# Kernel optimization log

Measured on AMD Instinct MI355X. Metric: run time of the kernel, lower is better.

Reference implementation:

```python
import jax, jax.numpy as jnp
import numpy as np

D_MODEL = 1024
N_HEADS = 16
D_K = D_MODEL // N_HEADS
D_FF = 4096
EPS = 1e-6


def setup_inputs() -> dict:
    key = jax.random.key(0)
    ks = jax.random.split(key, 12)
    s = 1.0 / np.sqrt(D_MODEL)
    inp = {
        "x": jax.random.normal(ks[0], (4, 2048, D_MODEL), jnp.float32),
        "src_mask": jnp.ones((4, 1, 1, 2048), jnp.int32),
        "Wq": jax.random.normal(ks[1], (D_MODEL, D_MODEL), jnp.float32) * s,
        "bq": jnp.zeros((D_MODEL,), jnp.float32),
        "Wk": jax.random.normal(ks[2], (D_MODEL, D_MODEL), jnp.float32) * s,
        "bk": jnp.zeros((D_MODEL,), jnp.float32),
        "Wv": jax.random.normal(ks[3], (D_MODEL, D_MODEL), jnp.float32) * s,
        "bv": jnp.zeros((D_MODEL,), jnp.float32),
        "Wo": jax.random.normal(ks[4], (D_MODEL, D_MODEL), jnp.float32) * s,
        "bo": jnp.zeros((D_MODEL,), jnp.float32),
        "W1": jax.random.normal(ks[5], (D_MODEL, D_FF), jnp.float32) * s,
        "b1": jnp.zeros((D_FF,), jnp.float32),
        "W2": jax.random.normal(ks[6], (D_FF, D_MODEL), jnp.float32) * (1.0 / np.sqrt(D_FF)),
        "b2": jnp.zeros((D_MODEL,), jnp.float32),
        # scalar LayerNormalization params (alpha=ones(1), bias=zeros(1)) for the 2 residual norms
        "ln1_alpha": jnp.ones((1,), jnp.float32),
        "ln1_bias": jnp.zeros((1,), jnp.float32),
        "ln2_alpha": jnp.ones((1,), jnp.float32),
        "ln2_bias": jnp.zeros((1,), jnp.float32),
    }
    return inp


def _layernorm(x, alpha, bias):
    # matches torch: mean + std (unbiased, ddof=1), (x-mean)/(std+eps)
    mean = jnp.mean(x, axis=-1, keepdims=True)
    std = jnp.std(x, axis=-1, keepdims=True, ddof=1)
    return alpha * ((x - mean) / (std + EPS)) + bias


def _mha(x, mask, Wq, bq, Wk, bk, Wv, bv, Wo, bo):
    B, S, _ = x.shape
    q = (x @ Wq + bq).reshape(B, S, N_HEADS, D_K).transpose(0, 2, 1, 3)
    k = (x @ Wk + bk).reshape(B, S, N_HEADS, D_K).transpose(0, 2, 1, 3)
    v = (x @ Wv + bv).reshape(B, S, N_HEADS, D_K).transpose(0, 2, 1, 3)
    scores = jnp.einsum("bhqd,bhkd->bhqk", q, k) / jnp.sqrt(jnp.float32(D_K))
    scores = jnp.where(mask == 0, jnp.float32(-1e9), scores)
    attn = jax.nn.softmax(scores, axis=-1)
    ctx = jnp.einsum("bhqk,bhkd->bhqd", attn, v)
    ctx = ctx.transpose(0, 2, 1, 3).reshape(B, S, D_MODEL)
    return ctx @ Wo + bo


def reference(x, src_mask, Wq, bq, Wk, bk, Wv, bv, Wo, bo, W1, b1, W2, b2,
              ln1_alpha, ln1_bias, ln2_alpha, ln2_bias):
    # pre-norm residual 1: self-attention
    h = _layernorm(x, ln1_alpha, ln1_bias)
    x = x + _mha(h, src_mask, Wq, bq, Wk, bk, Wv, bv, Wo, bo)
    # pre-norm residual 2: FFN
    h = _layernorm(x, ln2_alpha, ln2_bias)
    ff = jax.nn.relu(h @ W1 + b1) @ W2 + b2
    return x + ff
```

## Files before the change

### kernel.cpp

```cpp
#include <hip/hip_runtime.h>

typedef __attribute__((ext_vector_type(8))) short v8s;
typedef __attribute__((ext_vector_type(8))) unsigned short v8u;
typedef __attribute__((ext_vector_type(4))) unsigned short v4u;
typedef __attribute__((ext_vector_type(4))) float f32x4;

#define DEV __device__ __forceinline__

DEV unsigned short f2bf(float f) {
  union { float f; unsigned u; } v; v.f = f;
  unsigned r = v.u + 0x7fffu + ((v.u >> 16) & 1u);
  return (unsigned short)(r >> 16);
}

DEV float fexp2(float x) {
  float r; asm("v_exp_f32 %0, %1" : "=v"(r) : "v"(x)); return r;
}

DEV void gload16(const unsigned short* g, unsigned short* l) {
  __builtin_amdgcn_global_load_lds(
      (const __attribute__((address_space(1))) unsigned int*)g,
      (__attribute__((address_space(3))) unsigned int*)l, 16, 0, 0);
}

#define SL2E 0.1803368801111204f

__global__ __launch_bounds__(256) void ln_kernel(
    const float* __restrict__ x, unsigned short* __restrict__ h,
    const float* __restrict__ alpha, const float* __restrict__ beta)
{
  int row = blockIdx.x;
  int tid = threadIdx.x;
  const float4* xr = reinterpret_cast<const float4*>(x + (size_t)row * 1024);
  float4 v = xr[tid];
  float s  = v.x + v.y + v.z + v.w;
  float ss = v.x * v.x + v.y * v.y + v.z * v.z + v.w * v.w;
#pragma unroll
  for (int off = 1; off < 64; off <<= 1) {
    s  += __shfl_xor(s, off);
    ss += __shfl_xor(ss, off);
  }
  __shared__ float ps[4][2];
  int wid = tid >> 6, lane = tid & 63;
  if (lane == 0) { ps[wid][0] = s; ps[wid][1] = ss; }
  __syncthreads();
  s  = ps[0][0] + ps[1][0] + ps[2][0] + ps[3][0];
  ss = ps[0][1] + ps[1][1] + ps[2][1] + ps[3][1];
  float mean = s * (1.0f / 1024.0f);
  float var  = (ss - 1024.0f * mean * mean) * (1.0f / 1023.0f);
  float inv  = 1.0f / (sqrtf(fmaxf(var, 0.0f)) + 1e-6f);
  float a = alpha[0], b = beta[0];
  v4u o;
  o[0] = f2bf(a * ((v.x - mean) * inv) + b);
  o[1] = f2bf(a * ((v.y - mean) * inv) + b);
  o[2] = f2bf(a * ((v.z - mean) * inv) + b);
  o[3] = f2bf(a * ((v.w - mean) * inv) + b);
  *reinterpret_cast<v4u*>(h + (size_t)row * 1024 + tid * 4) = o;
}

__global__ __launch_bounds__(256) void transpose_convert(
    const float* __restrict__ W, unsigned short* __restrict__ Wt, int K, int N)
{
  __shared__ float t[32][33];
  int n0 = blockIdx.x * 32, k0 = blockIdx.y * 32;
  int tx = threadIdx.x, ty = threadIdx.y;
#pragma unroll
  for (int i = 0; i < 4; ++i)
    t[ty + i * 8][tx] = W[(size_t)(k0 + ty + i * 8) * N + n0 + tx];
  __syncthreads();
#pragma unroll
  for (int i = 0; i < 4; ++i)
    Wt[(size_t)(n0 + ty + i * 8) * K + k0 + tx] = f2bf(t[tx][ty + i * 8]);
}

#define BUF_ELEMS ((128 + 256) * 64)

DEV void stage_part(const unsigned short* Aptr, const unsigned short* Bptr,
                    unsigned short* buf, int K, int part, int wid, int lane)
{
  {
    int d = (part * 8 + wid) * 64 + lane;
    int r = d >> 3, p = d & 7;
    gload16(Aptr + (size_t)r * K + 8 * (p ^ (r & 7)),
            buf + (size_t)(part * 8 + wid) * 512);
  }
#pragma unroll
  for (int j = 0; j < 2; ++j) {
    int ib = part * 2 + j;
    int d = (ib * 8 + wid) * 64 + lane;
    int r = d >> 3, p = d & 7;
    gload16(Bptr + (size_t)r * K + 8 * (p ^ (r & 7)),
            buf + 128 * 64 + (size_t)(ib * 8 + wid) * 512);
  }
}

__global__ __launch_bounds__(512, 1) void gemm_qkv(
    const unsigned short* __restrict__ A, const unsigned short* __restrict__ Bt,
    const float* __restrict__ bq, const float* __restrict__ bk2,
    const float* __restrict__ bv,
    unsigned short* __restrict__ oq, unsigned short* __restrict__ ok2,
    unsigned short* __restrict__ ov, int M, int N, int K)
{
  __shared__ unsigned short lds[3 * BUF_ELEMS];

  int nbx = M >> 7, nwg = gridDim.x;
  int lin = blockIdx.x;
  int qq = nwg >> 3, rr = nwg & 7;
  int xcd = lin & 7, idx = lin >> 3;
  int swz = (xcd < rr ? xcd * (qq + 1) : rr * (qq + 1) + (xcd - rr) * qq) + idx;
  int bx = swz % nbx, by = swz / nbx;

  int tid = threadIdx.x, lane = tid & 63, wid = tid >> 6;
  int g = lane >> 4, c0 = lane & 15;
  int rowBase = bx * 128, colBase = by * 256;

  const unsigned short* Ab = A  + (size_t)rowBase * K;
  const unsigned short* Bb = Bt + (size_t)colBase * K;
  int NT = K >> 6;

  f32x4 acc[8][2];
#pragma unroll
  for (int m = 0; m < 8; ++m)
#pragma unroll
    for (int n = 0; n < 2; ++n) acc[m][n] = (f32x4){0.f, 0.f, 0.f, 0.f};

  stage_part(Ab, Bb, lds, K, 0, wid, lane);
  stage_part(Ab, Bb, lds, K, 1, wid, lane);
  stage_part(Ab + 64, Bb + 64, lds + BUF_ELEMS, K, 0, wid, lane);
  stage_part(Ab + 64, Bb + 64, lds + BUF_ELEMS, K, 1, wid, lane);
  asm volatile("s_waitcnt vmcnt(6)" ::: "memory");
  __builtin_amdgcn_s_barrier();
  asm volatile("" ::: "memory");

  int cur = 0;
  for (int t = 0; t < NT; ++t) {
    const char* Abuf = (const char*)(lds + cur * BUF_ELEMS);
    const char* Bbuf = Abuf + 128 * 128;
    int nxt2 = cur + 2; if (nxt2 >= 3) nxt2 -= 3;
    unsigned short* sbuf = lds + nxt2 * BUF_ELEMS;
    bool doStage = (t + 2 < NT);
    int ks_ = (t + 2) << 6;

#pragma unroll
    for (int ph = 0; ph < 2; ++ph) {
      v8s af[8], bfr[2];
#pragma unroll
      for (int m = 0; m < 8; ++m) {
        int row = m * 16 + c0;
        af[m] = *reinterpret_cast<const v8s*>(
            Abuf + row * 128 + ((ph * 64 + g * 16) ^ ((row & 7) << 4)));
      }
#pragma unroll
      for (int n = 0; n < 2; ++n) {
        int row = wid * 32 + n * 16 + c0;
        bfr[n] = *reinterpret_cast<const v8s*>(
            Bbuf + row * 128 + ((ph * 64 + g * 16) ^ ((row & 7) << 4)));
      }

      if (doStage) stage_part(Ab + ks_, Bb + ks_, sbuf, K, ph, wid, lane);

      __builtin_amdgcn_s_setprio(1);
#pragma unroll
      for (int m = 0; m < 8; ++m)
#pragma unroll
        for (int n = 0; n < 2; ++n)
          acc[m][n] = __builtin_amdgcn_mfma_f32_16x16x32_bf16(
              af[m], bfr[n], acc[m][n], 0, 0, 0);
      __builtin_amdgcn_s_setprio(0);
    }

    if (doStage)            asm volatile("s_waitcnt vmcnt(6)" ::: "memory");
    else if (t + 1 < NT)    asm volatile("s_waitcnt vmcnt(0)" ::: "memory");
    __builtin_amdgcn_sched_barrier(0);
    __builtin_amdgcn_s_barrier();
    asm volatile("" ::: "memory");
    cur = cur + 1; if (cur >= 3) cur -= 3;
  }

#pragma unroll
  for (int mf = 0; mf < 8; ++mf) {
#pragma unroll
    for (int nf = 0; nf < 2; ++nf) {
#pragma unroll
      for (int r = 0; r < 4; ++r) {
        int row = rowBase + mf * 16 + g * 4 + r;
        int col = colBase + wid * 32 + nf * 16 + c0;
        int sect = colBase >> 10;
        int cs = col & 1023;
        const float* bp = sect == 0 ? bq : (sect == 1 ? bk2 : bv);
        float v = acc[mf][nf][r] + bp[cs];
        int hh = cs >> 6, d = cs & 63;
        int b = row >> 11, sI = row & 2047;
        size_t bh = (size_t)(b * 16 + hh);
        if (sect == 0) {
          oq[(bh * 2048 + sI) * 64 + d] = f2bf(v * SL2E);
        } else if (sect == 1) {
          ok2[(bh * 2048 + sI) * 64 + d] = f2bf(v);
        } else {
          int k6 = sI & 63;
          int slot = ((k6 >> 5) << 5) | (((k6 >> 2) & 3) << 3) |
                     (((k6 >> 4) & 1) << 2) | (k6 & 3);
          int e2 = slot ^ ((d & 7) << 3);
          ov[((bh * 32 + (sI >> 6)) * 64 + d) * 64 + e2] = f2bf(v);
        }
      }
    }
  }
}

__global__ __launch_bounds__(512, 1) void gemm_ffn1_256(
    const unsigned short* __restrict__ A, const unsigned short* __restrict__ Bt,
    const float* __restrict__ bias, unsigned short* __restrict__ out,
    int M, int N, int K)
{
  __shared__ unsigned short lds[2][512 * 64];

  int nbx = M >> 8, nwg = gridDim.x;
  int lin = blockIdx.x;
  int qq = nwg >> 3, rr = nwg & 7;
  int xcd = lin & 7, idx = lin >> 3;
  int swz = (xcd < rr ? xcd * (qq + 1) : rr * (qq + 1) + (xcd - rr) * qq) + idx;
  int bx = swz % nbx, by = swz / nbx;

  int tid = threadIdx.x, lane = tid & 63, wid = tid >> 6;
  int wm = wid >> 2, wn = wid & 3;
  int g = lane >> 4, c0 = lane & 15;
  int rowBase = bx * 256, colBase = by * 256;

  const unsigned short* Ab = A  + (size_t)rowBase * K;
  const unsigned short* Bb = Bt + (size_t)colBase * K;
  int NT = K >> 6;

  const unsigned short* src[8]; int dq[8];
#pragma unroll
  for (int i = 0; i < 8; ++i) {
    int q = i * 512 + tid;
    dq[i] = q;
    if (i < 4) {
      int r = q >> 3, p = q & 7;
      src[i] = Ab + (size_t)r * K + 8 * (p ^ (r & 7));
    } else {
      int qb2 = q - 2048, r = qb2 >> 3, p = qb2 & 7;
      src[i] = Bb + (size_t)r * K + 8 * (p ^ (r & 7));
    }
  }

  f32x4 acc[8][4];
#pragma unroll
  for (int m = 0; m < 8; ++m)
#pragma unroll
    for (int n = 0; n < 4; ++n) acc[m][n] = (f32x4){0.f, 0.f, 0.f, 0.f};

#define STG256(tt, lo, hi) do { \
    unsigned short* sb_ = &lds[(tt) & 1][0]; int ko_ = (tt) << 6; \
    _Pragma("unroll") for (int i = lo; i < hi; ++i) gload16(src[i] + ko_, sb_ + dq[i] * 8); \
  } while (0)

  STG256(0, 0, 8);
  asm volatile("s_waitcnt vmcnt(0)" ::: "memory");
  __builtin_amdgcn_s_barrier();
  asm volatile("" ::: "memory");

  for (int t = 0; t < NT; ++t) {
    const char* buf = (const char*)&lds[t & 1][0];
    bool more = (t + 1 < NT);

#pragma unroll
    for (int ph = 0; ph < 2; ++ph) {
      v8s af[8], bfr[4];
#pragma unroll
      for (int m = 0; m < 8; ++m) {
        int row = wm * 128 + m * 16 + c0;
        af[m] = *reinterpret_cast<const v8s*>(
            buf + row * 128 + ((ph * 64 + g * 16) ^ ((row & 7) << 4)));
      }
#pragma unroll
      for (int n = 0; n < 4; ++n) {
        int row = wn * 64 + n * 16 + c0;
        bfr[n] = *reinterpret_cast<const v8s*>(
            buf + 32768 + row * 128 + ((ph * 64 + g * 16) ^ ((row & 7) << 4)));
      }

      if (more) { if (ph == 0) STG256(t + 1, 0, 4); else STG256(t + 1, 4, 8); }

      __builtin_amdgcn_s_setprio(1);
#pragma unroll
      for (int m = 0; m < 8; ++m)
#pragma unroll
        for (int n = 0; n < 4; ++n)
          acc[m][n] = __builtin_amdgcn_mfma_f32_16x16x32_bf16(
              af[m], bfr[n], acc[m][n], 0, 0, 0);
      __builtin_amdgcn_s_setprio(0);
    }

    if (more) asm volatile("s_waitcnt vmcnt(0)" ::: "memory");
    __builtin_amdgcn_sched_barrier(0);
    __builtin_amdgcn_s_barrier();
    asm volatile("" ::: "memory");
  }
#undef STG256

#pragma unroll
  for (int mf = 0; mf < 8; ++mf) {
#pragma unroll
    for (int nf = 0; nf < 4; ++nf) {
#pragma unroll
      for (int r = 0; r < 4; ++r) {
        int row = rowBase + wm * 128 + mf * 16 + g * 4 + r;
        int col = colBase + wn * 64 + nf * 16 + c0;
        float v = acc[mf][nf][r] + bias[col];
        out[(size_t)row * N + col] = f2bf(fmaxf(v, 0.0f));
      }
    }
  }
}

__global__ __launch_bounds__(512, 1) void gemm_pipe_res(
    const unsigned short* __restrict__ A, const unsigned short* __restrict__ Bt,
    const float* __restrict__ bias0, const float* __restrict__ resid,
    float* __restrict__ o0, int M, int N, int K)
{
  __shared__ unsigned short lds[3 * BUF_ELEMS];

  int nbx = M >> 7, nwg = gridDim.x;
  int lin = blockIdx.x;
  int qq = nwg >> 3, rr = nwg & 7;
  int xcd = lin & 7, idx = lin >> 3;
  int swz = (xcd < rr ? xcd * (qq + 1) : rr * (qq + 1) + (xcd - rr) * qq) + idx;
  int bx = swz % nbx, by = swz / nbx;

  int tid = threadIdx.x, lane = tid & 63, wid = tid >> 6;
  int g = lane >> 4, c0 = lane & 15;
  int rowBase = bx * 128, colBase = by * 256;

  const unsigned short* Ab = A  + (size_t)rowBase * K;
  const unsigned short* Bb = Bt + (size_t)colBase * K;
  int NT = K >> 6;

  f32x4 acc[8][2];
#pragma unroll
  for (int m = 0; m < 8; ++m)
#pragma unroll
    for (int n = 0; n < 2; ++n) acc[m][n] = (f32x4){0.f, 0.f, 0.f, 0.f};

  stage_part(Ab, Bb, lds, K, 0, wid, lane);
  stage_part(Ab, Bb, lds, K, 1, wid, lane);
  stage_part(Ab + 64, Bb + 64, lds + BUF_ELEMS, K, 0, wid, lane);
  stage_part(Ab + 64, Bb + 64, lds + BUF_ELEMS, K, 1, wid, lane);
  asm volatile("s_waitcnt vmcnt(6)" ::: "memory");
  __builtin_amdgcn_s_barrier();
  asm volatile("" ::: "memory");

  int cur = 0;
  for (int t = 0; t < NT; ++t) {
    const char* Abuf = (const char*)(lds + cur * BUF_ELEMS);
    const char* Bbuf = Abuf + 128 * 128;
    int nxt2 = cur + 2; if (nxt2 >= 3) nxt2 -= 3;
    unsigned short* sbuf = lds + nxt2 * BUF_ELEMS;
    bool doStage = (t + 2 < NT);
    int ks_ = (t + 2) << 6;

#pragma unroll
    for (int ph = 0; ph < 2; ++ph) {
      v8s af[8], bfr[2];
#pragma unroll
      for (int m = 0; m < 8; ++m) {
        int row = m * 16 + c0;
        af[m] = *reinterpret_cast<const v8s*>(
            Abuf + row * 128 + ((ph * 64 + g * 16) ^ ((row & 7) << 4)));
      }
#pragma unroll
      for (int n = 0; n < 2; ++n) {
        int row = wid * 32 + n * 16 + c0;
        bfr[n] = *reinterpret_cast<const v8s*>(
            Bbuf + row * 128 + ((ph * 64 + g * 16) ^ ((row & 7) << 4)));
      }

      if (doStage) stage_part(Ab + ks_, Bb + ks_, sbuf, K, ph, wid, lane);

      __builtin_amdgcn_s_setprio(1);
#pragma unroll
      for (int m = 0; m < 8; ++m)
#pragma unroll
        for (int n = 0; n < 2; ++n)
          acc[m][n] = __builtin_amdgcn_mfma_f32_16x16x32_bf16(
              af[m], bfr[n], acc[m][n], 0, 0, 0);
      __builtin_amdgcn_s_setprio(0);
    }

    if (doStage)            asm volatile("s_waitcnt vmcnt(6)" ::: "memory");
    else if (t + 1 < NT)    asm volatile("s_waitcnt vmcnt(0)" ::: "memory");
    __builtin_amdgcn_sched_barrier(0);
    __builtin_amdgcn_s_barrier();
    asm volatile("" ::: "memory");
    cur = cur + 1; if (cur >= 3) cur -= 3;
  }

#pragma unroll
  for (int mf = 0; mf < 8; ++mf) {
#pragma unroll
    for (int nf = 0; nf < 2; ++nf) {
#pragma unroll
      for (int r = 0; r < 4; ++r) {
        int row = rowBase + mf * 16 + g * 4 + r;
        int col = colBase + wid * 32 + nf * 16 + c0;
        float v = acc[mf][nf][r] + bias0[col];
        o0[(size_t)row * N + col] = resid[(size_t)row * N + col] + v;
      }
    }
  }
}

__global__ __launch_bounds__(256, 2) void attn_kernel(
    const unsigned short* __restrict__ q, const unsigned short* __restrict__ k,
    const unsigned short* __restrict__ vP, const int* __restrict__ mask,
    unsigned short* __restrict__ ctx)
{
  const int S = 2048, DK = 64, NT = 32;
  int bh = blockIdx.x;
  int b = bh >> 4, hh = bh & 15;
  int qbase = blockIdx.y * 256;
  int tid = threadIdx.x, lane = tid & 63, wid = tid >> 6;
  int g = lane >> 4, c0 = lane & 15;

  __shared__ unsigned short Ks[3 * 4096];
  __shared__ unsigned short Vs[3 * 4096];
  __shared__ unsigned short Mb[2048];

  const unsigned short* qb  = q  + (size_t)bh * S * DK;
  const unsigned short* kb  = k  + (size_t)bh * S * DK;
  const unsigned short* vPb = vP + (size_t)bh * 32 * 4096;
  const int* mb = mask + b * S;

  const int4* mb4 = reinterpret_cast<const int4*>(mb);
  int4 ma = mb4[tid * 2], mc = mb4[tid * 2 + 1];
  unsigned short bneg = f2bf(-1e9f);
  v8u bw;
  bw[0] = ma.x ? 0 : bneg; bw[1] = ma.y ? 0 : bneg;
  bw[2] = ma.z ? 0 : bneg; bw[3] = ma.w ? 0 : bneg;
  bw[4] = mc.x ? 0 : bneg; bw[5] = mc.y ? 0 : bneg;
  bw[6] = mc.z ? 0 : bneg; bw[7] = mc.w ? 0 : bneg;
  *reinterpret_cast<v8u*>(&Mb[tid * 8]) = bw;
  int okm = (ma.x && ma.y && ma.z && ma.w && mc.x && mc.y && mc.z && mc.w) ? 1 : 0;
  int allValid = __syncthreads_and(okm);

  int qrow = qbase + wid * 64 + c0;
  v8s aq[4][2];
#pragma unroll
  for (int s = 0; s < 4; ++s)
#pragma unroll
    for (int t = 0; t < 2; ++t)
      aq[s][t] = *reinterpret_cast<const v8s*>(
          &qb[(size_t)(qrow + s * 16) * DK + t * 32 + g * 8]);

  int i0 = tid, i1 = tid + 256;
  int r0 = i0 >> 3, m0 = i0 & 7;
  int r1 = i1 >> 3, m1 = i1 & 7;
  int ko0 = r0 * DK + 8 * (m0 ^ (r0 & 7));
  int ko1 = r1 * DK + 8 * (m1 ^ (r1 & 7));

  f32x4 acc[4][4], accl[4];
#pragma unroll
  for (int s = 0; s < 4; ++s) {
    accl[s] = (f32x4){0.f, 0.f, 0.f, 0.f};
#pragma unroll
    for (int no = 0; no < 4; ++no) acc[s][no] = (f32x4){0.f, 0.f, 0.f, 0.f};
  }
  v8s ones;
#pragma unroll
  for (int j = 0; j < 8; ++j) ones[j] = (short)0x3F80;

#define ASTAGE(bi, tt) do { \
    int tb_ = (tt) * 4096; \
    gload16(kb + tb_ + ko0, Ks + (bi) * 4096 + i0 * 8); \
    gload16(kb + tb_ + ko1, Ks + (bi) * 4096 + i1 * 8); \
    gload16(vPb + tb_ + i0 * 8, Vs + (bi) * 4096 + i0 * 8); \
    gload16(vPb + tb_ + i1 * 8, Vs + (bi) * 4096 + i1 * 8); \
  } while (0)

  ASTAGE(0, 0);
  ASTAGE(1, 1);
  asm volatile("s_waitcnt vmcnt(4)" ::: "memory");
  __builtin_amdgcn_s_barrier();
  asm volatile("" ::: "memory");

  int cur = 0, nx2 = 2;
  for (int t = 0; t < NT; ++t) {
    bool more2 = (t + 2 < NT);
    if (more2) ASTAGE(nx2, t + 2);
    const unsigned short* Kc = Ks + cur * 4096;
    const unsigned short* Vc = Vs + cur * 4096;

    v8s pb[4][2];
#pragma unroll
    for (int pp = 0; pp < 2; ++pp) {
      float pA[16], pB[16];
#pragma unroll
      for (int n = 0; n < 4; ++n) {
        int kvr = n * 16 + c0;
        const char* krow = (const char*)(Kc + kvr * DK);
        int sw = (kvr & 7) << 4;
        v8s ak0 = *reinterpret_cast<const v8s*>(krow + ((g * 16) ^ sw));
        v8s ak1 = *reinterpret_cast<const v8s*>(krow + ((64 + g * 16) ^ sw));
        f32x4 s0 = (f32x4){0.f, 0.f, 0.f, 0.f};
        f32x4 s1 = (f32x4){0.f, 0.f, 0.f, 0.f};
        s0 = __builtin_amdgcn_mfma_f32_16x16x32_bf16(ak0, aq[pp * 2][0], s0, 0, 0, 0);
        s0 = __builtin_amdgcn_mfma_f32_16x16x32_bf16(ak1, aq[pp * 2][1], s0, 0, 0, 0);
        s1 = __builtin_amdgcn_mfma_f32_16x16x32_bf16(ak0, aq[pp * 2 + 1][0], s1, 0, 0, 0);
        s1 = __builtin_amdgcn_mfma_f32_16x16x32_bf16(ak1, aq[pp * 2 + 1][1], s1, 0, 0, 0);
#pragma unroll
        for (int r = 0; r < 4; ++r) { pA[n * 4 + r] = s0[r]; pB[n * 4 + r] = s1[r]; }
      }
      if (!allValid) {
#pragma unroll
        for (int n = 0; n < 4; ++n) {
          v4u mbv = *reinterpret_cast<const v4u*>(&Mb[t * 64 + n * 16 + g * 4]);
#pragma unroll
          for (int r = 0; r < 4; ++r) {
            union { unsigned u; float f; } cv; cv.u = ((unsigned)mbv[r]) << 16;
            pA[n * 4 + r] += cv.f; pB[n * 4 + r] += cv.f;
          }
        }
      }
#pragma unroll
      for (int i = 0; i < 16; ++i) { pA[i] = fexp2(pA[i]); pB[i] = fexp2(pB[i]); }
#pragma unroll
      for (int c = 0; c < 2; ++c) {
        union { v8s s; unsigned u[4]; } kA, kB;
#pragma unroll
        for (int hp = 0; hp < 4; ++hp) {
          asm("v_cvt_pk_bf16_f32 %0, %1, %2"
              : "=v"(kA.u[hp]) : "v"(pA[c * 8 + 2 * hp]), "v"(pA[c * 8 + 2 * hp + 1]));
          asm("v_cvt_pk_bf16_f32 %0, %1, %2"
              : "=v"(kB.u[hp]) : "v"(pB[c * 8 + 2 * hp]), "v"(pB[c * 8 + 2 * hp + 1]));
        }
        pb[pp * 2][c] = kA.s; pb[pp * 2 + 1][c] = kB.s;
      }
    }

    __builtin_amdgcn_s_setprio(1);
#pragma unroll
    for (int c = 0; c < 2; ++c) {
#pragma unroll
      for (int no = 0; no < 4; ++no) {
        int d = no * 16 + c0;
        v8s av = *reinterpret_cast<const v8s*>(
            (const char*)(Vc + d * 64) + ((c * 64 + g * 16) ^ ((d & 7) << 4)));
#pragma unroll
        for (int s = 0; s < 4; ++s)
          acc[s][no] = __builtin_amdgcn_mfma_f32_16x16x32_bf16(av, pb[s][c], acc[s][no], 0, 0, 0);
      }
#pragma unroll
      for (int s = 0; s < 4; ++s)
        accl[s] = __builtin_amdgcn_mfma_f32_16x16x32_bf16(ones, pb[s][c], accl[s], 0, 0, 0);
    }
    __builtin_amdgcn_s_setprio(0);

    if (more2)              asm volatile("s_waitcnt vmcnt(4)" ::: "memory");
    else if (t + 1 < NT)    asm volatile("s_waitcnt vmcnt(0)" ::: "memory");
    __builtin_amdgcn_sched_barrier(0);
    __builtin_amdgcn_s_barrier();
    asm volatile("" ::: "memory");
    cur = (cur + 1 < 3) ? cur + 1 : 0;
    nx2 = (nx2 + 1 < 3) ? nx2 + 1 : 0;
  }
#undef ASTAGE

#pragma unroll
  for (int s = 0; s < 4; ++s) {
    float inv = 1.0f / fmaxf(accl[s][0], 1e-30f);
#pragma unroll
    for (int no = 0; no < 4; ++no) {
      v4u o;
      o[0] = f2bf(acc[s][no][0] * inv);
      o[1] = f2bf(acc[s][no][1] * inv);
      o[2] = f2bf(acc[s][no][2] * inv);
      o[3] = f2bf(acc[s][no][3] * inv);
      *reinterpret_cast<v4u*>(
          &ctx[(size_t)(b * S + qrow + s * 16) * 1024 + hh * 64 + no * 16 + g * 4]) = o;
    }
  }
}

extern "C" void kernel_launch(void* const* d_in, const int* in_sizes, int n_in,
                              void* d_out, int out_size, void* d_ws, size_t ws_size,
                              hipStream_t stream)
{
  (void)in_sizes; (void)n_in; (void)out_size; (void)ws_size;
  const float* x    = (const float*)d_in[0];
  const int*   mask = (const int*)d_in[1];
  const float* Wq = (const float*)d_in[2];  const float* bq = (const float*)d_in[3];
  const float* Wk = (const float*)d_in[4];  const float* bk = (const float*)d_in[5];
  const float* Wv = (const float*)d_in[6];  const float* bv = (const float*)d_in[7];
  const float* Wo = (const float*)d_in[8];  const float* bo = (const float*)d_in[9];
  const float* W1 = (const float*)d_in[10]; const float* b1 = (const float*)d_in[11];
  const float* W2 = (const float*)d_in[12]; const float* b2 = (const float*)d_in[13];
  const float* ln1a = (const float*)d_in[14]; const float* ln1b = (const float*)d_in[15];
  const float* ln2a = (const float*)d_in[16]; const float* ln2b = (const float*)d_in[17];

  char* ws = (char*)d_ws;
  const size_t MB = (size_t)1 << 20;
  unsigned short* wqkvT = (unsigned short*)(ws + 0 * MB);
  unsigned short* woT = (unsigned short*)(ws + 6 * MB);
  unsigned short* w1T = (unsigned short*)(ws + 8 * MB);
  unsigned short* w2T = (unsigned short*)(ws + 16 * MB);
  unsigned short* hb  = (unsigned short*)(ws + 24 * MB);
  unsigned short* qb  = (unsigned short*)(ws + 40 * MB);
  unsigned short* kb  = (unsigned short*)(ws + 56 * MB);
  unsigned short* vPb = (unsigned short*)(ws + 72 * MB);
  unsigned short* ctx = (unsigned short*)(ws + 88 * MB);
  unsigned short* gb  = (unsigned short*)(ws + 40 * MB);
  float* xout = (float*)d_out;

  dim3 tb(32, 8);
  transpose_convert<<<dim3(32, 32),  tb, 0, stream>>>(Wq, wqkvT,               1024, 1024);
  transpose_convert<<<dim3(32, 32),  tb, 0, stream>>>(Wk, wqkvT + 1024 * 1024, 1024, 1024);
  transpose_convert<<<dim3(32, 32),  tb, 0, stream>>>(Wv, wqkvT + 2048 * 1024, 1024, 1024);
  transpose_convert<<<dim3(32, 32),  tb, 0, stream>>>(Wo, woT, 1024, 1024);
  transpose_convert<<<dim3(128, 32), tb, 0, stream>>>(W1, w1T, 1024, 4096);
  transpose_convert<<<dim3(32, 128), tb, 0, stream>>>(W2, w2T, 4096, 1024);

  ln_kernel<<<8192, 256, 0, stream>>>(x, hb, ln1a, ln1b);

  gemm_qkv<<<768, 512, 0, stream>>>(hb, wqkvT, bq, bk, bv, qb, kb, vPb, 8192, 3072, 1024);

  attn_kernel<<<dim3(64, 8), 256, 0, stream>>>(qb, kb, vPb, mask, ctx);

  gemm_pipe_res<<<256, 512, 0, stream>>>(ctx, woT, bo, x, xout, 8192, 1024, 1024);

  ln_kernel<<<8192, 256, 0, stream>>>(xout, hb, ln2a, ln2b);

  gemm_ffn1_256<<<512, 512, 0, stream>>>(hb, w1T, b1, gb, 8192, 4096, 1024);

  gemm_pipe_res<<<256, 512, 0, stream>>>(gb, w2T, b2, xout, xout, 8192, 1024, 4096);
}
```

Before: 368.9 us.

## Use 256x256 tiles for QKV GEMM and split-K FFN2 with combine kernel

Generalizes the 256x256-tile FFN1 GEMM into a templated kernel and uses it for the QKV projection, replacing the 128x256 triple-buffered kernel and halving the grid. The FFN2 GEMM becomes a two-way split-K over 256 workgroups, writing bf16 partials. A separate elementwise kernel then adds the partials, the bias and the residual. This is meant to raise per-tile data reuse and fill the device better for the small-N FFN2 GEMM. The cost is an extra kernel launch, extra partial-sum traffic, and rounding of the partial sums to bf16.

```diff
diff --git a/kernel.cpp b/kernel.cpp
--- a/kernel.cpp
+++ b/kernel.cpp
@@ -11,6 +11,10 @@
   union { float f; unsigned u; } v; v.f = f;
   unsigned r = v.u + 0x7fffu + ((v.u >> 16) & 1u);
   return (unsigned short)(r >> 16);
+}
+
+DEV float bf2f(unsigned short s) {
+  union { unsigned u; float f; } v; v.u = ((unsigned)s) << 16; return v.f;
 }
 
 DEV float fexp2(float x) {
@@ -73,145 +77,15 @@
     Wt[(size_t)(n0 + ty + i * 8) * K + k0 + tx] = f2bf(t[tx][ty + i * 8]);
 }
 
-#define BUF_ELEMS ((128 + 256) * 64)
-
-DEV void stage_part(const unsigned short* Aptr, const unsigned short* Bptr,
-                    unsigned short* buf, int K, int part, int wid, int lane)
-{
-  {
-    int d = (part * 8 + wid) * 64 + lane;
-    int r = d >> 3, p = d & 7;
-    gload16(Aptr + (size_t)r * K + 8 * (p ^ (r & 7)),
-            buf + (size_t)(part * 8 + wid) * 512);
-  }
-#pragma unroll
-  for (int j = 0; j < 2; ++j) {
-    int ib = part * 2 + j;
-    int d = (ib * 8 + wid) * 64 + lane;
-    int r = d >> 3, p = d & 7;
-    gload16(Bptr + (size_t)r * K + 8 * (p ^ (r & 7)),
-            buf + 128 * 64 + (size_t)(ib * 8 + wid) * 512);
-  }
-}
-
-__global__ __launch_bounds__(512, 1) void gemm_qkv(
+enum { MODE_QKV = 0, MODE_FFN1 = 3, MODE_PART = 4 };
+
+template <int MODE>
+__global__ __launch_bounds__(512, 1) void gemm_256s(
     const unsigned short* __restrict__ A, const unsigned short* __restrict__ Bt,
-    const float* __restrict__ bq, const float* __restrict__ bk2,
-    const float* __restrict__ bv,
-    unsigned short* __restrict__ oq, unsigned short* __restrict__ ok2,
-    unsigned short* __restrict__ ov, int M, int N, int K)
-{
-  __shared__ unsigned short lds[3 * BUF_ELEMS];
-
-  int nbx = M >> 7, nwg = gridDim.x;
-  int lin = blockIdx.x;
-  int qq = nwg >> 3, rr = nwg & 7;
-  int xcd = lin & 7, idx = lin >> 3;
-  int swz = (xcd < rr ? xcd * (qq + 1) : rr * (qq + 1) + (xcd - rr) * qq) + idx;
-  int bx = swz % nbx, by = swz / nbx;
-
-  int tid = threadIdx.x, lane = tid & 63, wid = tid >> 6;
-  int g = lane >> 4, c0 = lane & 15;
-  int rowBase = bx * 128, colBase = by * 256;
-
-  const unsigned short* Ab = A  + (size_t)rowBase * K;
-  const unsigned short* Bb = Bt + (size_t)colBase * K;
-  int NT = K >> 6;
-
-  f32x4 acc[8][2];
-#pragma unroll
-  for (int m = 0; m < 8; ++m)
-#pragma unroll
-    for (int n = 0; n < 2; ++n) acc[m][n] = (f32x4){0.f, 0.f, 0.f, 0.f};
-
-  stage_part(Ab, Bb, lds, K, 0, wid, lane);
-  stage_part(Ab, Bb, lds, K, 1, wid, lane);
-  stage_part(Ab + 64, Bb + 64, lds + BUF_ELEMS, K, 0, wid, lane);
-  stage_part(Ab + 64, Bb + 64, lds + BUF_ELEMS, K, 1, wid, lane);
-  asm volatile("s_waitcnt vmcnt(6)" ::: "memory");
-  __builtin_amdgcn_s_barrier();
-  asm volatile("" ::: "memory");
-
-  int cur = 0;
-  for (int t = 0; t < NT; ++t) {
-    const char* Abuf = (const char*)(lds + cur * BUF_ELEMS);
-    const char* Bbuf = Abuf + 128 * 128;
-    int nxt2 = cur + 2; if (nxt2 >= 3) nxt2 -= 3;
-    unsigned short* sbuf = lds + nxt2 * BUF_ELEMS;
-    bool doStage = (t + 2 < NT);
-    int ks_ = (t + 2) << 6;
-
-#pragma unroll
-    for (int ph = 0; ph < 2; ++ph) {
-      v8s af[8], bfr[2];
-#pragma unroll
-      for (int m = 0; m < 8; ++m) {
-        int row = m * 16 + c0;
-        af[m] = *reinterpret_cast<const v8s*>(
-            Abuf + row * 128 + ((ph * 64 + g * 16) ^ ((row & 7) << 4)));
-      }
-#pragma unroll
-      for (int n = 0; n < 2; ++n) {
-        int row = wid * 32 + n * 16 + c0;
-        bfr[n] = *reinterpret_cast<const v8s*>(
-            Bbuf + row * 128 + ((ph * 64 + g * 16) ^ ((row & 7) << 4)));
-      }
-
-      if (doStage) stage_part(Ab + ks_, Bb + ks_, sbuf, K, ph, wid, lane);
-
-      __builtin_amdgcn_s_setprio(1);
-#pragma unroll
-      for (int m = 0; m < 8; ++m)
-#pragma unroll
-        for (int n = 0; n < 2; ++n)
-          acc[m][n] = __builtin_amdgcn_mfma_f32_16x16x32_bf16(
-              af[m], bfr[n], acc[m][n], 0, 0, 0);
-      __builtin_amdgcn_s_setprio(0);
-    }
-
-    if (doStage)            asm volatile("s_waitcnt vmcnt(6)" ::: "memory");
-    else if (t + 1 < NT)    asm volatile("s_waitcnt vmcnt(0)" ::: "memory");
-    __builtin_amdgcn_sched_barrier(0);
-    __builtin_amdgcn_s_barrier();
-    asm volatile("" ::: "memory");
-    cur = cur + 1; if (cur >= 3) cur -= 3;
-  }
-
-#pragma unroll
-  for (int mf = 0; mf < 8; ++mf) {
-#pragma unroll
-    for (int nf = 0; nf < 2; ++nf) {
-#pragma unroll
-      for (int r = 0; r < 4; ++r) {
-        int row = rowBase + mf * 16 + g * 4 + r;
-        int col = colBase + wid * 32 + nf * 16 + c0;
-        int sect = colBase >> 10;
-        int cs = col & 1023;
-        const float* bp = sect == 0 ? bq : (sect == 1 ? bk2 : bv);
-        float v = acc[mf][nf][r] + bp[cs];
-        int hh = cs >> 6, d = cs & 63;
-        int b = row >> 11, sI = row & 2047;
-        size_t bh = (size_t)(b * 16 + hh);
-        if (sect == 0) {
-          oq[(bh * 2048 + sI) * 64 + d] = f2bf(v * SL2E);
-        } else if (sect == 1) {
-          ok2[(bh * 2048 + sI) * 64 + d] = f2bf(v);
-        } else {
-          int k6 = sI & 63;
-          int slot = ((k6 >> 5) << 5) | (((k6 >> 2) & 3) << 3) |
-                     (((k6 >> 4) & 1) << 2) | (k6 & 3);
-          int e2 = slot ^ ((d & 7) << 3);
-          ov[((bh * 32 + (sI >> 6)) * 64 + d) * 64 + e2] = f2bf(v);
-        }
-      }
-    }
-  }
-}
-
-__global__ __launch_bounds__(512, 1) void gemm_ffn1_256(
-    const unsigned short* __restrict__ A, const unsigned short* __restrict__ Bt,
-    const float* __restrict__ bias, unsigned short* __restrict__ out,
-    int M, int N, int K)
+    const float* __restrict__ bias0, const float* __restrict__ bias1,
+    const float* __restrict__ bias2,
+    void* __restrict__ o0, void* __restrict__ o1, void* __restrict__ o2,
+    int M, int N, int K, int KRUN)
 {
   __shared__ unsigned short lds[2][512 * 64];
 
@@ -220,16 +94,23 @@
   int qq = nwg >> 3, rr = nwg & 7;
   int xcd = lin & 7, idx = lin >> 3;
   int swz = (xcd < rr ? xcd * (qq + 1) : rr * (qq + 1) + (xcd - rr) * qq) + idx;
-  int bx = swz % nbx, by = swz / nbx;
+
+  int bx, by, kbase;
+  if constexpr (MODE == MODE_PART) {
+    int h = swz >> 7, s2 = swz & 127;
+    bx = s2 % nbx; by = s2 / nbx; kbase = h * KRUN;
+  } else {
+    bx = swz % nbx; by = swz / nbx; kbase = 0;
+  }
 
   int tid = threadIdx.x, lane = tid & 63, wid = tid >> 6;
   int wm = wid >> 2, wn = wid & 3;
   int g = lane >> 4, c0 = lane & 15;
   int rowBase = bx * 256, colBase = by * 256;
 
-  const unsigned short* Ab = A  + (size_t)rowBase * K;
-  const unsigned short* Bb = Bt + (size_t)colBase * K;
-  int NT = K >> 6;
+  const unsigned short* Ab = A  + (size_t)rowBase * K + kbase;
+  const unsigned short* Bb = Bt + (size_t)colBase * K + kbase;
+  int NT = KRUN >> 6;
 
   const unsigned short* src[8]; int dq[8];
 #pragma unroll
@@ -308,10 +189,74 @@
       for (int r = 0; r < 4; ++r) {
         int row = rowBase + wm * 128 + mf * 16 + g * 4 + r;
         int col = colBase + wn * 64 + nf * 16 + c0;
-        float v = acc[mf][nf][r] + bias[col];
-        out[(size_t)row * N + col] = f2bf(fmaxf(v, 0.0f));
-      }
-    }
+        float v = acc[mf][nf][r];
+        if constexpr (MODE == MODE_QKV) {
+          int sect = colBase >> 10;
+          int cs = col & 1023;
+          const float* bp = sect == 0 ? bias0 : (sect == 1 ? bias1 : bias2);
+          v += bp[cs];
+          int hh = cs >> 6, d = cs & 63;
+          int b = row >> 11, sI = row & 2047;
+          size_t bh = (size_t)(b * 16 + hh);
+          if (sect == 0) {
+            ((unsigned short*)o0)[(bh * 2048 + sI) * 64 + d] = f2bf(v * SL2E);
+          } else if (sect == 1) {
+            ((unsigned short*)o1)[(bh * 2048 + sI) * 64 + d] = f2bf(v);
+          } else {
+            int k6 = sI & 63;
+            int slot = ((k6 >> 5) << 5) | (((k6 >> 2) & 3) << 3) |
+                       (((k6 >> 4) & 1) << 2) | (k6 & 3);
+            int e2 = slot ^ ((d & 7) << 3);
+            ((unsigned short*)o2)[((bh * 32 + (sI >> 6)) * 64 + d) * 64 + e2] = f2bf(v);
+          }
+        } else if constexpr (MODE == MODE_FFN1) {
+          v += bias0[col];
+          ((unsigned short*)o0)[(size_t)row * N + col] = f2bf(fmaxf(v, 0.0f));
+        } else {
+          unsigned short* po = (kbase == 0) ? (unsigned short*)o0 : (unsigned short*)o1;
+          po[(size_t)row * N + col] = f2bf(v);
+        }
+      }
+    }
+  }
+}
+
+__global__ __launch_bounds__(256) void ffn2_combine(
+    const unsigned short* __restrict__ p0, const unsigned short* __restrict__ p1,
+    const float* __restrict__ b2, float* __restrict__ xout)
+{
+  size_t off = ((size_t)blockIdx.x * 256 + threadIdx.x) * 4;
+  int col = (int)(off & 1023);
+  float4 xv = *reinterpret_cast<const float4*>(xout + off);
+  v4u a = *reinterpret_cast<const v4u*>(p0 + off);
+  v4u b = *reinterpret_cast<const v4u*>(p1 + off);
+  float4 bb = *reinterpret_cast<const float4*>(b2 + col);
+  float4 o;
+  o.x = xv.x + bb.x + bf2f(a[0]) + bf2f(b[0]);
+  o.y = xv.y + bb.y + bf2f(a[1]) + bf2f(b[1]);
+  o.z = xv.z + bb.z + bf2f(a[2]) + bf2f(b[2]);
+  o.w = xv.w + bb.w + bf2f(a[3]) + bf2f(b[3]);
+  *reinterpret_cast<float4*>(xout + off) = o;
+}
+
+#define BUF_ELEMS ((128 + 256) * 64)
+
+DEV void stage_part(const unsigned short* Aptr, const unsigned short* Bptr,
+                    unsigned short* buf, int K, int part, int wid, int lane)
+{
+  {
+    int d = (part * 8 + wid) * 64 + lane;
+    int r = d >> 3, p = d & 7;
+    gload16(Aptr + (size_t)r * K + 8 * (p ^ (r & 7)),
+            buf + (size_t)(part * 8 + wid) * 512);
+  }
+#pragma unroll
+  for (int j = 0; j < 2; ++j) {
+    int ib = part * 2 + j;
+    int d = (ib * 8 + wid) * 64 + lane;
+    int r = d >> 3, p = d & 7;
+    gload16(Bptr + (size_t)r * K + 8 * (p ^ (r & 7)),
+            buf + 128 * 64 + (size_t)(ib * 8 + wid) * 512);
   }
 }
 
@@ -601,10 +546,12 @@
   char* ws = (char*)d_ws;
   const size_t MB = (size_t)1 << 20;
   unsigned short* wqkvT = (unsigned short*)(ws + 0 * MB);
+  unsigned short* p1  = (unsigned short*)(ws + 0 * MB);
   unsigned short* woT = (unsigned short*)(ws + 6 * MB);
   unsigned short* w1T = (unsigned short*)(ws + 8 * MB);
   unsigned short* w2T = (unsigned short*)(ws + 16 * MB);
   unsigned short* hb  = (unsigned short*)(ws + 24 * MB);
+  unsigned short* p0  = (unsigned short*)(ws + 24 * MB);
   unsigned short* qb  = (unsigned short*)(ws + 40 * MB);
   unsigned short* kb  = (unsigned short*)(ws + 56 * MB);
   unsigned short* vPb = (unsigned short*)(ws + 72 * MB);
@@ -622,7 +569,8 @@
 
   ln_kernel<<<8192, 256, 0, stream>>>(x, hb, ln1a, ln1b);
 
-  gemm_qkv<<<768, 512, 0, stream>>>(hb, wqkvT, bq, bk, bv, qb, kb, vPb, 8192, 3072, 1024);
+  gemm_256s<MODE_QKV><<<384, 512, 0, stream>>>(
+      hb, wqkvT, bq, bk, bv, qb, kb, vPb, 8192, 3072, 1024, 1024);
 
   attn_kernel<<<dim3(64, 8), 256, 0, stream>>>(qb, kb, vPb, mask, ctx);
 
@@ -630,7 +578,11 @@
 
   ln_kernel<<<8192, 256, 0, stream>>>(xout, hb, ln2a, ln2b);
 
-  gemm_ffn1_256<<<512, 512, 0, stream>>>(hb, w1T, b1, gb, 8192, 4096, 1024);
-
-  gemm_pipe_res<<<256, 512, 0, stream>>>(gb, w2T, b2, xout, xout, 8192, 1024, 4096);
-}
+  gemm_256s<MODE_FFN1><<<512, 512, 0, stream>>>(
+      hb, w1T, b1, nullptr, nullptr, gb, nullptr, nullptr, 8192, 4096, 1024, 1024);
+
+  gemm_256s<MODE_PART><<<256, 512, 0, stream>>>(
+      gb, w2T, nullptr, nullptr, nullptr, p0, p1, nullptr, 8192, 1024, 4096, 2048);
+
+  ffn2_combine<<<8192, 256, 0, stream>>>(p0, p1, b2, xout);
+}
```

Measured after the change: 386.4 us. 4.7% more time.
